# Kernel optimization log

Measured on AMD Instinct MI355X. Metric: run time of the kernel, lower is better.

## Reference

```python
import jax, jax.numpy as jnp
import numpy as np

N = 65536    # cluster nodes
E = 1048576  # edges (~avg degree 16); first N are self-loops (asserted in original)
B = 32       # graphs in the batch
D = 64       # channels (hard-coded 64 in source)
NL = 4       # 4 stacked PointTransformerConv encoders
NC = 2       # classes (Linear(64, 2) in source)


def _mlp2(y, W1, b1, W2, b2):
    # PyG MLP(plain_last=False) in eval mode: Linear -> BN(identity at init) -> ReLU, twice
    return jax.nn.relu(jax.nn.relu(y @ W1 + b1) @ W2 + b2)


def _seg_softmax(a, dst, n):
    # channelwise softmax over incoming edges of each destination node
    m = jax.ops.segment_max(a, dst, num_segments=n)
    e = jnp.exp(a - m[dst])
    s = jax.ops.segment_sum(e, dst, num_segments=n)
    return e / s[dst]


def _pt_conv(x, pos, src, dst, Wl, Ws, Wd, pW1, pb1, pW2, pb2, aW1, ab1, aW2, ab2):
    # PyG PointTransformerConv (add_self_loops=False, default sum aggregation)
    n = x.shape[0]
    v = x @ Wl      # lin   -> value, gathered at src (x_j)
    a_s = x @ Ws    # lin_src -> alpha_j
    a_d = x @ Wd    # lin_dst -> alpha_i
    delta = _mlp2(pos[dst] - pos[src], pW1, pb1, pW2, pb2)            # pos_nn(pos_i - pos_j), [E, D]
    alpha = _mlp2(a_d[dst] - a_s[src] + delta, aW1, ab1, aW2, ab2)    # attn_nn(...), [E, D]
    alpha = _seg_softmax(alpha, dst, n)
    msg = alpha * (v[src] + delta)                                     # [E, D]
    return jax.ops.segment_sum(msg, dst, num_segments=n)               # [N, D]


def setup_inputs() -> dict:
    key = jax.random.key(0)
    ks = jax.random.split(key, 16)
    x = jax.random.normal(ks[0], (N, D), dtype=jnp.float32)
    pos = jax.random.uniform(ks[1], (N, 2), dtype=jnp.float32)
    src = jax.random.randint(ks[2], (E,), 0, N)
    dst = jax.random.randint(ks[3], (E,), 0, N)
    loops = jnp.arange(N)
    src = src.at[:N].set(loops)  # guarantee self-loops
    dst = dst.at[:N].set(loops)
    edge_index = jnp.stack([src, dst]).astype(jnp.int32)
    batch = ((jnp.arange(N) * B) // N).astype(jnp.int32)  # sorted graph ids, every graph non-empty
    s = jnp.float32(0.05)
    def rn(k, shape):
        return jax.random.normal(k, shape, dtype=jnp.float32) * s
    return {
        'x': x, 'pos': pos,
        'W_lin': rn(ks[4], (NL, D, D)),
        'W_src': rn(ks[5], (NL, D, D)),
        'W_dst': rn(ks[6], (NL, D, D)),
        'pos_W1': rn(ks[7], (NL, 2, D)),
        'pos_b1': jnp.zeros((NL, D), jnp.float32),
        'pos_W2': rn(ks[8], (NL, D, D)),
        'pos_b2': jnp.zeros((NL, D), jnp.float32),
        'attn_W1': rn(ks[9], (NL, D, D)),
        'attn_b1': jnp.zeros((NL, D), jnp.float32),
        'attn_W2': rn(ks[10], (NL, D, D)),
        'attn_b2': jnp.zeros((NL, D), jnp.float32),
        'out_W': rn(ks[11], (D, NC)),
        'out_b': jnp.zeros((NC,), jnp.float32),
        'edge_index': edge_index,
        'batch': batch,
    }


def reference(x, pos, W_lin, W_src, W_dst, pos_W1, pos_b1, pos_W2, pos_b2,
              attn_W1, attn_b1, attn_W2, attn_b2, out_W, out_b, edge_index, batch):
    src, dst = edge_index[0], edge_index[1]
    h = x
    for i in range(NL):  # 4 stacked cluster encoders (fixed layer count)
        h = _pt_conv(h, pos, src, dst, W_lin[i], W_src[i], W_dst[i],
                     pos_W1[i], pos_b1[i], pos_W2[i], pos_b2[i],
                     attn_W1[i], attn_b1[i], attn_W2[i], attn_b2[i])
    g = jax.ops.segment_max(h, batch, num_segments=B)  # global_max_pool -> [B, D]
    return g @ out_W + out_b                           # [B, NC]
```

## Files before the change

kernel.cpp:

```cpp
#include <hip/hip_runtime.h>
#include <hip/hip_bf16.h>
#include <math.h>

#define N_NODES 65536
#define N_EDGES 1048576
#define NB      32
#define D       64
#define NLAYERS 4
#define G       16
#define CH      32
#define AST     72
#define PST     68

typedef __attribute__((ext_vector_type(8))) short short8;
typedef __attribute__((ext_vector_type(4))) float f32x4;

__device__ __forceinline__ float relu_f(float x){ return x > 0.f ? x : 0.f; }
__device__ __forceinline__ unsigned short bfbits(float x){
    __bf16 h = (__bf16)x;
    return __builtin_bit_cast(unsigned short, h);
}
__device__ __forceinline__ float bfval(float x){
    __bf16 h = (__bf16)x;
    return (float)h;
}
__device__ __forceinline__ f32x4 mfma16(short8 a, short8 b, f32x4 c){
    return __builtin_amdgcn_mfma_f32_16x16x32_bf16(a, b, c, 0, 0, 0);
}


__global__ void k_zero(int* __restrict__ p){
    p[blockIdx.x * 256 + threadIdx.x] = 0;
}

__global__ void k_hist(const int* __restrict__ dst, int* __restrict__ deg){
    int e = blockIdx.x * 256 + threadIdx.x;
    if (e < N_EDGES) atomicAdd(&deg[dst[e]], 1);
}

__global__ void k_scan1(const int* __restrict__ deg, int* __restrict__ part, int* __restrict__ bsum){
    __shared__ int s[256];
    int t = threadIdx.x;
    int i = blockIdx.x * 256 + t;
    int v = deg[i];
    s[t] = v; __syncthreads();
    for (int ofs = 1; ofs < 256; ofs <<= 1){
        int tv = (t >= ofs) ? s[t - ofs] : 0;
        __syncthreads();
        s[t] += tv;
        __syncthreads();
    }
    part[i] = s[t] - v;
    if (t == 255) bsum[blockIdx.x] = s[255];
}

__global__ void k_scan2(const int* __restrict__ bsum, int* __restrict__ bofs){
    __shared__ int s[256];
    int t = threadIdx.x;
    int v = bsum[t];
    s[t] = v; __syncthreads();
    for (int ofs = 1; ofs < 256; ofs <<= 1){
        int tv = (t >= ofs) ? s[t - ofs] : 0;
        __syncthreads();
        s[t] += tv;
        __syncthreads();
    }
    bofs[t] = s[t] - v;
}

__global__ void k_scan3(const int* __restrict__ part, const int* __restrict__ bofs,
                        int* __restrict__ off, int* __restrict__ cursor){
    int i = blockIdx.x * 256 + threadIdx.x;
    int o = part[i] + bofs[i >> 8];
    off[i] = o; cursor[i] = o;
    if (i == 0) off[N_NODES] = N_EDGES;
}

__global__ void k_scatter(const int* __restrict__ ei, const float* __restrict__ pos,
                          int* __restrict__ cursor, int* __restrict__ srcs,
                          float* __restrict__ pdb){
    int e = blockIdx.x * 256 + threadIdx.x;
    if (e >= N_EDGES) return;
    int s = ei[e], d = ei[N_EDGES + e];
    int p = atomicAdd(&cursor[d], 1);
    srcs[p]    = s;
    pdb[2*p]   = pos[2*d]   - pos[2*s];
    pdb[2*p+1] = pos[2*d+1] - pos[2*s+1];
}


__global__ void k_pack(const float* __restrict__ pW2, const float* __restrict__ aW1,
                       const float* __restrict__ aW2, unsigned short* __restrict__ bpk){
    int b  = blockIdx.x;
    int kf = b & 1, nb = (b >> 1) & 3;
    int mat = (b >> 3) % 3, L = b / 24;
    int t = threadIdx.x;
    int lane = t & 63, jj = (t >> 6) * 2;
    const float* W = (mat == 0 ? pW2 : (mat == 1 ? aW1 : aW2)) + (size_t)L * D * D;
    int n = nb * 16 + (lane & 15);
    unsigned short* dsthi = bpk + (size_t)L * 24576
                          + (((size_t)mat * 4 + nb) * 2 + kf) * 512 + lane * 8 + jj;
    #pragma unroll
    for (int u = 0; u < 2; ++u){
        int j = jj + u;
        int k = kf * 32 + (lane >> 4) * 8 + j;
        float w = W[k * D + n];
        float hv = bfval(w);
        dsthi[u]         = bfbits(w);
        dsthi[12288 + u] = bfbits(w - hv);
    }
}


__global__ __launch_bounds__(256) void k_nodegemm(
    const float* __restrict__ h,
    const float* __restrict__ Wl, const float* __restrict__ Ws, const float* __restrict__ Wd,
    float* __restrict__ v, float* __restrict__ as_, float* __restrict__ ad)
{
    __shared__ float HT[D * 68];
    int row0 = blockIdx.x * 64;
    int t = threadIdx.x;
    {
        int r  = t >> 2;
        int kb = (t & 3) * 16;
        const float4* hp = (const float4*)(h + (size_t)(row0 + r) * D + kb);
        #pragma unroll
        for (int i4 = 0; i4 < 4; ++i4){
            float4 a = hp[i4];
            HT[(kb + i4*4 + 0)*68 + r] = a.x;
            HT[(kb + i4*4 + 1)*68 + r] = a.y;
            HT[(kb + i4*4 + 2)*68 + r] = a.z;
            HT[(kb + i4*4 + 3)*68 + r] = a.w;
        }
    }
    __syncthreads();
    int tr = t >> 4, tc = t & 15;
    int r0 = tr * 4, c0 = tc * 4;
    float accl[4][4] = {}, accs[4][4] = {}, accd[4][4] = {};
    #pragma unroll 8
    for (int k = 0; k < D; ++k){
        float4 a  = *(const float4*)&HT[k*68 + r0];
        float4 bl = *(const float4*)(Wl + k*D + c0);
        float4 bs = *(const float4*)(Ws + k*D + c0);
        float4 bd = *(const float4*)(Wd + k*D + c0);
        float av[4] = {a.x, a.y, a.z, a.w};
        #pragma unroll
        for (int i = 0; i < 4; ++i){
            accl[i][0] += av[i]*bl.x; accl[i][1] += av[i]*bl.y;
            accl[i][2] += av[i]*bl.z; accl[i][3] += av[i]*bl.w;
            accs[i][0] += av[i]*bs.x; accs[i][1] += av[i]*bs.y;
            accs[i][2] += av[i]*bs.z; accs[i][3] += av[i]*bs.w;
            accd[i][0] += av[i]*bd.x; accd[i][1] += av[i]*bd.y;
            accd[i][2] += av[i]*bd.z; accd[i][3] += av[i]*bd.w;
        }
    }
    #pragma unroll
    for (int i = 0; i < 4; ++i){
        size_t o = (size_t)(row0 + r0 + i) * D + c0;
        *(float4*)(v  + o) = make_float4(accl[i][0], accl[i][1], accl[i][2], accl[i][3]);
        *(float4*)(as_+ o) = make_float4(accs[i][0], accs[i][1], accs[i][2], accs[i][3]);
        *(float4*)(ad + o) = make_float4(accd[i][0], accd[i][1], accd[i][2], accd[i][3]);
    }
}


__device__ __forceinline__ void load_bfrag(const unsigned short* __restrict__ bpk,
                                           int g, int w, int lane,
                                           short8& Bh0, short8& Bh1,
                                           short8& Bl0, short8& Bl1)
{
    int bo = ((g*4 + w)*2)*512 + lane*8;
    asm volatile("" : "+v"(bo));
    Bh0 = __builtin_bit_cast(short8, *(const uint4*)(bpk + bo));
    Bh1 = __builtin_bit_cast(short8, *(const uint4*)(bpk + bo + 512));
    Bl0 = __builtin_bit_cast(short8, *(const uint4*)(bpk + 12288 + bo));
    Bl1 = __builtin_bit_cast(short8, *(const uint4*)(bpk + 12288 + bo + 512));
}

__device__ __forceinline__ void gemm_tile2(const unsigned short* __restrict__ Ah,
                                           const unsigned short* __restrict__ Al,
                                           short8 Bh0, short8 Bh1, short8 Bl0, short8 Bl1,
                                           int ln, int q, f32x4* accs)
{
    #pragma unroll
    for (int mt = 0; mt < 2; ++mt){
        int ro = (mt*16 + ln) * AST;
        short8 ah0 = __builtin_bit_cast(short8, *(const uint4*)(Ah + ro + q*8));
        short8 ah1 = __builtin_bit_cast(short8, *(const uint4*)(Ah + ro + 32 + q*8));
        short8 al0 = __builtin_bit_cast(short8, *(const uint4*)(Al + ro + q*8));
        short8 al1 = __builtin_bit_cast(short8, *(const uint4*)(Al + ro + 32 + q*8));
        f32x4 acc = {0.f, 0.f, 0.f, 0.f};
        acc = mfma16(ah0, Bh0, acc);
        acc = mfma16(ah1, Bh1, acc);
        acc = mfma16(al0, Bh0, acc);
        acc = mfma16(al1, Bh1, acc);
        acc = mfma16(ah0, Bl0, acc);
        acc = mfma16(ah1, Bl1, acc);
        accs[mt] = acc;
    }
}

__global__ __launch_bounds__(256) void k_edge(
    const int* __restrict__ off, const int* __restrict__ srcs, const float* __restrict__ pdb,
    const float* __restrict__ v, const float* __restrict__ as_, const float* __restrict__ ad,
    const float* __restrict__ pW1, const float* __restrict__ pb1, const float* __restrict__ pb2,
    const float* __restrict__ ab1, const float* __restrict__ ab2,
    const unsigned short* __restrict__ bpk,
    float* __restrict__ hout)
{
    __shared__ __align__(16) unsigned short ALDS[2 * CH * AST];
    __shared__ __align__(16) unsigned short ULDS[2 * CH * AST];
    __shared__ int s_sp[CH];
    __shared__ int s_off[20];

    unsigned short* Ahi = ALDS;
    unsigned short* Alo = ALDS + CH * AST;
    unsigned short* Uhi = ULDS;
    unsigned short* Ulo = ULDS + CH * AST;
    float* Pf  = (float*)ULDS;
    float* PMf = (float*)ALDS;

    int t  = threadIdx.x;
    int n0 = blockIdx.x * G;
    if (t <= G) s_off[t] = off[n0 + t];
    __syncthreads();
    int e_begin = s_off[0], e_end = s_off[G];

    int w = t >> 6, lane = t & 63;
    int q = lane >> 4, ln = lane & 15;
    int c = w * 16 + ln;

    float pb2c = pb2[c], ab1c = ab1[c], ab2c = ab2[c];

    float den[4] = {0.f, 0.f, 0.f, 0.f};
    float num[4] = {0.f, 0.f, 0.f, 0.f};

    for (int ec = e_begin; ec < e_end; ec += CH){
        int cnt = min(CH, e_end - ec);
        {
            int e8 = t >> 3, kb = (t & 7) * 8;
            int g = ec + ((e8 < cnt) ? e8 : 0);
            if (t < CH){
                int gg = ec + ((t < cnt) ? t : 0);
                int s = srcs[gg];
                int l = 0;
                while (l < G-1 && gg >= s_off[l+1]) ++l;
                s_sp[t] = s | (l << 16);
            }
            float2 pd = *(const float2*)(pdb + 2*g);
            float p0 = pd.x, p1 = pd.y;
            unsigned int hw[4], lw[4];
            #pragma unroll
            for (int i2 = 0; i2 < 4; ++i2){
                int k = kb + i2*2;
                float f0 = relu_f(fmaf(p1, pW1[D + k],     fmaf(p0, pW1[k],     pb1[k])));
                float f1 = relu_f(fmaf(p1, pW1[D + k + 1], fmaf(p0, pW1[k + 1], pb1[k + 1])));
                unsigned short h0 = bfbits(f0), h1 = bfbits(f1);
                float r0f = f0 - bfval(f0), r1f = f1 - bfval(f1);
                unsigned short l0 = bfbits(r0f), l1 = bfbits(r1f);
                hw[i2] = (unsigned int)h0 | ((unsigned int)h1 << 16);
                lw[i2] = (unsigned int)l0 | ((unsigned int)l1 << 16);
            }
            *(uint4*)&Ahi[e8*AST + kb] = make_uint4(hw[0], hw[1], hw[2], hw[3]);
            *(uint4*)&Alo[e8*AST + kb] = make_uint4(lw[0], lw[1], lw[2], lw[3]);
        }
        __syncthreads();
        float Mreg[8];
        {
            short8 Bh0, Bh1, Bl0, Bl1;
            load_bfrag(bpk, 0, w, lane, Bh0, Bh1, Bl0, Bl1);
            float pa[8];
            unsigned int dnp = 0;
            #pragma unroll
            for (int mt = 0; mt < 2; ++mt)
                #pragma unroll
                for (int r = 0; r < 4; ++r){
                    int i = mt*4 + r;
                    int e = mt*16 + q*4 + r;
                    int sp = s_sp[e];
                    int s  = sp & 0xFFFF;
                    dnp |= (unsigned int)(sp >> 16) << (4*i);
                    Mreg[i] = v  [(size_t)s * D + c];
                    pa[i]   = as_[(size_t)s * D + c];
                }
            #pragma unroll
            for (int mt = 0; mt < 2; ++mt){
                int ro = (mt*16 + ln) * AST;
                short8 ah0 = __builtin_bit_cast(short8, *(const uint4*)(Ahi + ro + q*8));
                short8 ah1 = __builtin_bit_cast(short8, *(const uint4*)(Ahi + ro + 32 + q*8));
                short8 al0 = __builtin_bit_cast(short8, *(const uint4*)(Alo + ro + q*8));
                short8 al1 = __builtin_bit_cast(short8, *(const uint4*)(Alo + ro + 32 + q*8));
                f32x4 acc = {0.f, 0.f, 0.f, 0.f};
                acc = mfma16(ah0, Bh0, acc);
                acc = mfma16(ah1, Bh1, acc);
                acc = mfma16(al0, Bh0, acc);
                acc = mfma16(al1, Bh1, acc);
                acc = mfma16(ah0, Bl0, acc);
                acc = mfma16(ah1, Bl1, acc);
                #pragma unroll
                for (int r = 0; r < 4; ++r){
                    int i = mt*4 + r;
                    int e = mt*16 + q*4 + r;
                    float dlt = relu_f(acc[r] + pb2c);
                    int dn = n0 + (int)((dnp >> (4*i)) & 15u);
                    float vd = ad[(size_t)dn * D + c];
                    float uu = vd - pa[i] + dlt;
                    Mreg[i] += dlt;
                    Uhi[e*AST + c] = bfbits(uu);
                    Ulo[e*AST + c] = bfbits(uu - bfval(uu));
                }
            }
        }
        __syncthreads();
        {
            short8 Bh0, Bh1, Bl0, Bl1;
            load_bfrag(bpk, 1, w, lane, Bh0, Bh1, Bl0, Bl1);
            f32x4 accs[2];
            gemm_tile2(Uhi, Ulo, Bh0, Bh1, Bl0, Bl1, ln, q, accs);
            #pragma unroll
            for (int mt = 0; mt < 2; ++mt){
                #pragma unroll
                for (int r = 0; r < 4; ++r){
                    int e = mt*16 + q*4 + r;
                    float t2 = relu_f(accs[mt][r] + ab1c);
                    Ahi[e*AST + c] = bfbits(t2);
                    Alo[e*AST + c] = bfbits(t2 - bfval(t2));
                }
            }
        }
        __syncthreads();
        {
            short8 Bh0, Bh1, Bl0, Bl1;
            load_bfrag(bpk, 2, w, lane, Bh0, Bh1, Bl0, Bl1);
            f32x4 accs[2];
            gemm_tile2(Ahi, Alo, Bh0, Bh1, Bl0, Bl1, ln, q, accs);
            #pragma unroll
            for (int mt = 0; mt < 2; ++mt){
                #pragma unroll
                for (int r = 0; r < 4; ++r){
                    int e = mt*16 + q*4 + r;
                    float a = relu_f(accs[mt][r] + ab2c);
                    float p = __expf(a);
                    accs[mt][r] = p;
                    Pf[e*PST + c] = p;
                }
            }
            __syncthreads();
            #pragma unroll
            for (int mt = 0; mt < 2; ++mt){
                #pragma unroll
                for (int r = 0; r < 4; ++r){
                    int e = mt*16 + q*4 + r;
                    PMf[e*PST + c] = accs[mt][r] * Mreg[mt*4 + r];
                }
            }
        }
        __syncthreads();
        #pragma unroll
        for (int qn = 0; qn < 4; ++qn){
            int l  = w*4 + qn;
            int gs = max(s_off[l], ec);
            int ge = min(s_off[l+1], ec + cnt);
            float dd = den[qn], nn = num[qn];
            for (int g = gs; g < ge; ++g){
                int e = g - ec;
                dd += Pf [e*PST + lane];
                nn += PMf[e*PST + lane];
            }
            den[qn] = dd; num[qn] = nn;
        }
        __syncthreads();
    }
    #pragma unroll
    for (int qn = 0; qn < 4; ++qn){
        int n = n0 + w*4 + qn;
        hout[(size_t)n * D + lane] = num[qn] / den[qn];
    }
}


__global__ __launch_bounds__(256) void k_pool(const float* __restrict__ h,
                                              const float* __restrict__ outW,
                                              const float* __restrict__ outb,
                                              float* __restrict__ out)
{
    __shared__ float sm[4][64];
    __shared__ float sp[2][64];
    int b = blockIdx.x;
    int t = threadIdx.x, j = t & 63, g = t >> 6;
    float mx = -1e30f;
    for (int r = b*2048 + g; r < (b+1)*2048; r += 4)
        mx = fmaxf(mx, h[(size_t)r * D + j]);
    sm[g][j] = mx;
    __syncthreads();
    if (t < 64){
        float m = fmaxf(fmaxf(sm[0][j], sm[1][j]), fmaxf(sm[2][j], sm[3][j]));
        sp[0][j] = m * outW[j*2 + 0];
        sp[1][j] = m * outW[j*2 + 1];
    }
    __syncthreads();
    if (t == 0){
        float s0 = outb[0], s1 = outb[1];
        for (int k = 0; k < 64; ++k){ s0 += sp[0][k]; s1 += sp[1][k]; }
        out[b*2]   = s0;
        out[b*2+1] = s1;
    }
}


extern "C" void kernel_launch(void* const* d_in, const int* in_sizes, int n_in,
                              void* d_out, int out_size, void* d_ws, size_t ws_size,
                              hipStream_t stream)
{
    const float* x    = (const float*)d_in[0];
    const float* pos  = (const float*)d_in[1];
    const float* Wl   = (const float*)d_in[2];
    const float* Ws   = (const float*)d_in[3];
    const float* Wd   = (const float*)d_in[4];
    const float* pW1  = (const float*)d_in[5];
    const float* pb1  = (const float*)d_in[6];
    const float* pW2  = (const float*)d_in[7];
    const float* pb2  = (const float*)d_in[8];
    const float* aW1  = (const float*)d_in[9];
    const float* ab1  = (const float*)d_in[10];
    const float* aW2  = (const float*)d_in[11];
    const float* ab2  = (const float*)d_in[12];
    const float* outW = (const float*)d_in[13];
    const float* outb = (const float*)d_in[14];
    const int*   ei   = (const int*)d_in[15];
    float* out = (float*)d_out;

    char* wp = (char*)d_ws;
    auto alloc = [&](size_t bytes){
        void* p = (void*)wp;
        wp += (bytes + 255) & ~(size_t)255;
        return p;
    };
    int*   deg    = (int*)  alloc((size_t)N_NODES * 4);
    int*   part   = (int*)  alloc((size_t)N_NODES * 4);
    int*   bsum   = (int*)  alloc(1024);
    int*   bofs   = (int*)  alloc(1024);
    int*   off    = (int*)  alloc((size_t)(N_NODES + 1) * 4);
    int*   cursor = (int*)  alloc((size_t)N_NODES * 4);
    int*   srcs   = (int*)  alloc((size_t)N_EDGES * 4);
    float* pdb    = (float*)alloc((size_t)N_EDGES * 8);
    float* vv     = (float*)alloc((size_t)N_NODES * D * 4);
    float* as_    = (float*)alloc((size_t)N_NODES * D * 4);
    float* ad     = (float*)alloc((size_t)N_NODES * D * 4);
    float* h0     = (float*)alloc((size_t)N_NODES * D * 4);
    float* h1     = (float*)alloc((size_t)N_NODES * D * 4);
    unsigned short* bpk = (unsigned short*)alloc((size_t)NLAYERS * 24576 * 2);

    k_zero   <<<256,  256, 0, stream>>>(deg);
    k_hist   <<<4096, 256, 0, stream>>>(ei + N_EDGES, deg);
    k_scan1  <<<256,  256, 0, stream>>>(deg, part, bsum);
    k_scan2  <<<1,    256, 0, stream>>>(bsum, bofs);
    k_scan3  <<<256,  256, 0, stream>>>(part, bofs, off, cursor);
    k_scatter<<<4096, 256, 0, stream>>>(ei, pos, cursor, srcs, pdb);
    k_pack   <<<96,   256, 0, stream>>>(pW2, aW1, aW2, bpk);

    const float* hin = x;
    float* hbuf[2] = { h0, h1 };
    for (int L = 0; L < NLAYERS; ++L){
        float* hout = hbuf[L & 1];
        k_nodegemm<<<N_NODES/64, 256, 0, stream>>>(hin,
            Wl + (size_t)L*D*D, Ws + (size_t)L*D*D, Wd + (size_t)L*D*D,
            vv, as_, ad);
        k_edge<<<N_NODES/G, 256, 0, stream>>>(off, srcs, pdb, vv, as_, ad,
            pW1 + (size_t)L*2*D, pb1 + (size_t)L*D, pb2 + (size_t)L*D,
            ab1 + (size_t)L*D, ab2 + (size_t)L*D,
            bpk + (size_t)L*24576,
            hout);
        hin = hout;
    }
    k_pool<<<NB, 256, 0, stream>>>(hin, outW, outb, out);
}
```

Measured before the change: 1.545 ms.

## Software-prefetch next chunk's gathered v and a_src rows into registers

Each 32-edge chunk's source-indexed gathers of v and a_src are now issued one chunk ahead, right after the current chunk's first GEMM. The loads can then overlap the attention GEMM, softmax and aggregation stages instead of stalling the position-MLP stage. Each thread reads the source indices straight from global memory rather than through shared memory, and s_sp now holds only the local destination id. This costs 16 extra live registers per thread, which could lower occupancy.

```diff
diff --git a/kernel.cpp b/kernel.cpp
--- a/kernel.cpp
+++ b/kernel.cpp
@@ -200,6 +200,25 @@
     }
 }
 
+__device__ __forceinline__ void prefetch8(int ec2, int e_end, int q, int c,
+    const int* __restrict__ srcs, const float* __restrict__ v, const float* __restrict__ as_,
+    float* __restrict__ npv, float* __restrict__ npa)
+{
+    if (ec2 >= e_end) return;
+    int cnt2 = min(CH, e_end - ec2);
+    #pragma unroll
+    for (int mt = 0; mt < 2; ++mt)
+        #pragma unroll
+        for (int r = 0; r < 4; ++r){
+            int i = mt*4 + r;
+            int e = mt*16 + q*4 + r;
+            int g = ec2 + ((e < cnt2) ? e : 0);
+            int s = srcs[g];
+            npv[i] = v  [(size_t)s * D + c];
+            npa[i] = as_[(size_t)s * D + c];
+        }
+}
+
 __global__ __launch_bounds__(256) void k_edge(
     const int* __restrict__ off, const int* __restrict__ srcs, const float* __restrict__ pdb,
     const float* __restrict__ v, const float* __restrict__ as_, const float* __restrict__ ad,
@@ -235,6 +254,9 @@
     float den[4] = {0.f, 0.f, 0.f, 0.f};
     float num[4] = {0.f, 0.f, 0.f, 0.f};
 
+    float npv[8], npa[8];
+    prefetch8(e_begin, e_end, q, c, srcs, v, as_, npv, npa);
+
     for (int ec = e_begin; ec < e_end; ec += CH){
         int cnt = min(CH, e_end - ec);
         {
@@ -242,10 +264,9 @@
             int g = ec + ((e8 < cnt) ? e8 : 0);
             if (t < CH){
                 int gg = ec + ((t < cnt) ? t : 0);
-                int s = srcs[gg];
                 int l = 0;
                 while (l < G-1 && gg >= s_off[l+1]) ++l;
-                s_sp[t] = s | (l << 16);
+                s_sp[t] = l;
             }
             float2 pd = *(const float2*)(pdb + 2*g);
             float p0 = pd.x, p1 = pd.y;
@@ -269,7 +290,6 @@
         {
             short8 Bh0, Bh1, Bl0, Bl1;
             load_bfrag(bpk, 0, w, lane, Bh0, Bh1, Bl0, Bl1);
-            float pa[8];
             unsigned int dnp = 0;
             #pragma unroll
             for (int mt = 0; mt < 2; ++mt)
@@ -277,11 +297,7 @@
                 for (int r = 0; r < 4; ++r){
                     int i = mt*4 + r;
                     int e = mt*16 + q*4 + r;
-                    int sp = s_sp[e];
-                    int s  = sp & 0xFFFF;
-                    dnp |= (unsigned int)(sp >> 16) << (4*i);
-                    Mreg[i] = v  [(size_t)s * D + c];
-                    pa[i]   = as_[(size_t)s * D + c];
+                    dnp |= (unsigned int)s_sp[e] << (4*i);
                 }
             #pragma unroll
             for (int mt = 0; mt < 2; ++mt){
@@ -304,12 +320,13 @@
                     float dlt = relu_f(acc[r] + pb2c);
                     int dn = n0 + (int)((dnp >> (4*i)) & 15u);
                     float vd = ad[(size_t)dn * D + c];
-                    float uu = vd - pa[i] + dlt;
-                    Mreg[i] += dlt;
+                    float uu = vd - npa[i] + dlt;
+                    Mreg[i] = npv[i] + dlt;
                     Uhi[e*AST + c] = bfbits(uu);
                     Ulo[e*AST + c] = bfbits(uu - bfval(uu));
                 }
             }
+            prefetch8(ec + CH, e_end, q, c, srcs, v, as_, npv, npa);
         }
         __syncthreads();
         {
```

New measurement: 1.573 ms. No clear change (+1.8%).
